# Kernel tuning notes

Measured on AMD Instinct MI355X. Metric: run time of the kernel, lower is better.

## Reference

```python
import jax, jax.numpy as jnp
import numpy as np

PRIMES = (2, 3, 5, 7, 11, 13, 17, 19, 23, 29)
TEMP = 1000.0  # softmax_temperature
B, S = 32, 2048

def _templates(p):
    # circle template for residue r: (cos(2*pi*r/p), sin(2*pi*r/p)) -> [p, 2]
    ang = 2.0 * np.pi * np.arange(p) / p
    return jnp.asarray(np.stack([np.cos(ang), np.sin(ang)], axis=-1).astype(np.float32))

def _mul_onehot(p):
    # onehot[a, b, (a*b) % p] = 1 -> [p, p, p]
    t = (np.arange(p)[:, None] * np.arange(p)[None, :]) % p
    return jnp.asarray((t[..., None] == np.arange(p)).astype(np.float32))

TEMPLATES = [_templates(p) for p in PRIMES]
MUL_OH = [_mul_onehot(p) for p in PRIMES]

def setup_inputs() -> dict:
    key = jax.random.key(0)
    k1, k2 = jax.random.split(key)
    m = len(PRIMES)
    return {
        "a_circle": jax.random.normal(k1, (B, S, m, 2), dtype=jnp.float32),
        "b_circle": jax.random.normal(k2, (B, S, m, 2), dtype=jnp.float32),
    }

def _circle_add(a, b):
    # complex multiply: angles add -> (a + b) mod p on the circle
    ca, sa = a[..., 0], a[..., 1]
    cb, sb = b[..., 0], b[..., 1]
    return jnp.stack([ca * cb - sa * sb, sa * cb + ca * sb], axis=-1)

def _circle_sub(a, b):
    # a - b = a + conj(b): negate sin of b
    b_conj = jnp.stack([b[..., 0], -b[..., 1]], axis=-1)
    return _circle_add(a, b_conj)

def _decode_soft(c_i, tmpl):
    # c_i: [B, S, 2], tmpl: [p, 2] -> soft one-hot over residues [B, S, p]
    sim = jnp.einsum('bsd,pd->bsp', c_i, tmpl)
    return jax.nn.softmax(TEMP * sim, axis=-1)

def _circle_mul(a, b):
    outs = []
    for i, p in enumerate(PRIMES):
        tmpl = TEMPLATES[i]
        a_soft = _decode_soft(a[:, :, i, :], tmpl)
        b_soft = _decode_soft(b[:, :, i, :], tmpl)
        # outer product of soft residues contracted with mul table
        dist = jnp.einsum('bsi,bsj,ijk->bsk', a_soft, b_soft, MUL_OH[i])
        outs.append(dist @ tmpl)  # re-encode to circle: [B, S, 2]
    return jnp.stack(outs, axis=2)  # [B, S, m, 2]

def reference(a_circle, b_circle):
    add = _circle_add(a_circle, b_circle)
    sub = _circle_sub(a_circle, b_circle)
    mul = _circle_mul(a_circle, b_circle)
    return jnp.stack([add, sub, mul], axis=0)  # [3, B, S, m, 2]
```

## Files before the change

### kernel.cpp

```cpp
#include <hip/hip_runtime.h>


#define SOFTMAX_TEMP 1000.0f

constexpr double PI_D = 3.14159265358979323846264338327950288;

constexpr double tay_cos(double x) {
    double x2 = x * x, term = 1.0, sum = 1.0;
    for (int k = 1; k <= 15; ++k) { term *= -x2 / double((2 * k - 1) * (2 * k)); sum += term; }
    return sum;
}
constexpr double tay_sin(double x) {
    double x2 = x * x, term = x, sum = x;
    for (int k = 1; k <= 15; ++k) { term *= -x2 / double((2 * k) * (2 * k + 1)); sum += term; }
    return sum;
}

template <int P> struct Tab { float c[P]; float s[P]; };

template <int P>
constexpr Tab<P> make_tab() {
    Tab<P> t{};
    for (int r = 0; r < P; ++r) {
        double x = 2.0 * PI_D * double(r) / double(P);
        if (x > PI_D) x -= 2.0 * PI_D;
        t.c[r] = (float)tay_cos(x);
        t.s[r] = (float)tay_sin(x);
    }
    return t;
}

template <int P>
__device__ __forceinline__ void mul_prime(float ca, float sa, float cb, float sb,
                                          float& oc, float& os) {
    constexpr Tab<P> T = make_tab<P>();

    float ea[P], eb[P];
    float ma = -1e30f, mb = -1e30f;
#pragma unroll
    for (int r = 0; r < P; ++r) {
        float va = ca * T.c[r] + sa * T.s[r];
        float vb = cb * T.c[r] + sb * T.s[r];
        ea[r] = va; eb[r] = vb;
        ma = fmaxf(ma, va); mb = fmaxf(mb, vb);
    }
    float Sa = 0.f, Sb = 0.f;
#pragma unroll
    for (int r = 0; r < P; ++r) {
        float xa = __expf(SOFTMAX_TEMP * (ea[r] - ma));
        float xb = __expf(SOFTMAX_TEMP * (eb[r] - mb));
        ea[r] = xa; Sa += xa;
        eb[r] = xb; Sb += xb;
    }

    float W[P];
#pragma unroll
    for (int k = 0; k < P; ++k) W[k] = 0.f;
    W[0] = ea[0] * Sb + eb[0] * Sa - ea[0] * eb[0];
#pragma unroll
    for (int i = 1; i < P; ++i) {
#pragma unroll
        for (int j = 1; j < P; ++j) {
            const int k = (i * j) % P;
            W[k] = fmaf(ea[i], eb[j], W[k]);
        }
    }

    float accC = 0.f, accS = 0.f;
#pragma unroll
    for (int k = 0; k < P; ++k) {
        accC = fmaf(W[k], T.c[k], accC);
        accS = fmaf(W[k], T.s[k], accS);
    }
    float inv = 1.0f / (Sa * Sb);
    oc = accC * inv;
    os = accS * inv;
}

__global__ __launch_bounds__(640) void arith_kernel(const float* __restrict__ a,
                                                    const float* __restrict__ b,
                                                    float* __restrict__ out,
                                                    int n_pairs) {
    const int pair = blockIdx.x * 64 + threadIdx.x;
    const int pi = threadIdx.y;
    if (pair >= n_pairs) return;

    const int base = pair * 20 + pi * 2;
    const float2 av = *(const float2*)(a + base);
    const float2 bv = *(const float2*)(b + base);
    const float ca = av.x, sa = av.y, cb = bv.x, sb = bv.y;

    const float pcc = ca * cb, pss = sa * sb, psc = sa * cb, pcs = ca * sb;
    const int plane = n_pairs * 20;
    *(float2*)(out + base)          = make_float2(pcc - pss, psc + pcs);
    *(float2*)(out + plane + base)  = make_float2(pcc + pss, psc - pcs);

    float oc, os;
    switch (pi) {
        case 0: mul_prime<2>(ca, sa, cb, sb, oc, os); break;
        case 1: mul_prime<3>(ca, sa, cb, sb, oc, os); break;
        case 2: mul_prime<5>(ca, sa, cb, sb, oc, os); break;
        case 3: mul_prime<7>(ca, sa, cb, sb, oc, os); break;
        case 4: mul_prime<11>(ca, sa, cb, sb, oc, os); break;
        case 5: mul_prime<13>(ca, sa, cb, sb, oc, os); break;
        case 6: mul_prime<17>(ca, sa, cb, sb, oc, os); break;
        case 7: mul_prime<19>(ca, sa, cb, sb, oc, os); break;
        case 8: mul_prime<23>(ca, sa, cb, sb, oc, os); break;
        default: mul_prime<29>(ca, sa, cb, sb, oc, os); break;
    }
    *(float2*)(out + 2 * plane + base) = make_float2(oc, os);
}

extern "C" void kernel_launch(void* const* d_in, const int* in_sizes, int n_in,
                              void* d_out, int out_size, void* d_ws, size_t ws_size,
                              hipStream_t stream) {
    const float* a = (const float*)d_in[0];
    const float* b = (const float*)d_in[1];
    float* out = (float*)d_out;
    const int n_pairs = in_sizes[0] / 20;

    dim3 block(64, 10);
    dim3 grid((n_pairs + 63) / 64);
    arith_kernel<<<grid, block, 0, stream>>>(a, b, out, n_pairs);
}
```

Measured before the change: 75.95 us.

## Fuse softmax of a into product loop and regroup work into 256-thread blocks

Computes the exponentials of operand a on the fly inside the outer-product loop instead of storing them in an array, and recomputes logits rather than keeping them, which is meant to cut register pressure for large primes. The launch changes from 64x10 blocks to 256-thread blocks, where each 64-lane wavefront handles one (pair-group, prime) unit. This is intended to raise occupancy and scheduling flexibility, at the cost of some recomputed FMAs and extra index arithmetic.

```diff
diff --git a/kernel.cpp b/kernel.cpp
--- a/kernel.cpp
+++ b/kernel.cpp
@@ -35,36 +35,40 @@
                                           float& oc, float& os) {
     constexpr Tab<P> T = make_tab<P>();
 
-    float ea[P], eb[P];
     float ma = -1e30f, mb = -1e30f;
 #pragma unroll
     for (int r = 0; r < P; ++r) {
-        float va = ca * T.c[r] + sa * T.s[r];
-        float vb = cb * T.c[r] + sb * T.s[r];
-        ea[r] = va; eb[r] = vb;
-        ma = fmaxf(ma, va); mb = fmaxf(mb, vb);
+        ma = fmaxf(ma, ca * T.c[r] + sa * T.s[r]);
+        mb = fmaxf(mb, cb * T.c[r] + sb * T.s[r]);
     }
-    float Sa = 0.f, Sb = 0.f;
+
+    float eb[P];
+    float Sb = 0.f;
 #pragma unroll
     for (int r = 0; r < P; ++r) {
-        float xa = __expf(SOFTMAX_TEMP * (ea[r] - ma));
-        float xb = __expf(SOFTMAX_TEMP * (eb[r] - mb));
-        ea[r] = xa; Sa += xa;
-        eb[r] = xb; Sb += xb;
+        float x = __expf(SOFTMAX_TEMP * (cb * T.c[r] + sb * T.s[r] - mb));
+        eb[r] = x; Sb += x;
     }
 
     float W[P];
 #pragma unroll
     for (int k = 0; k < P; ++k) W[k] = 0.f;
-    W[0] = ea[0] * Sb + eb[0] * Sa - ea[0] * eb[0];
+
+    float Sa = 0.f, ea0 = 0.f;
 #pragma unroll
-    for (int i = 1; i < P; ++i) {
+    for (int i = 0; i < P; ++i) {
+        float ea_i = __expf(SOFTMAX_TEMP * (ca * T.c[i] + sa * T.s[i] - ma));
+        Sa += ea_i;
+        if (i == 0) { ea0 = ea_i; }
+        else {
 #pragma unroll
-        for (int j = 1; j < P; ++j) {
-            const int k = (i * j) % P;
-            W[k] = fmaf(ea[i], eb[j], W[k]);
+            for (int j = 1; j < P; ++j) {
+                const int k = (i * j) % P;
+                W[k] = fmaf(ea_i, eb[j], W[k]);
+            }
         }
     }
+    W[0] += ea0 * Sb + eb[0] * (Sa - ea0);
 
     float accC = 0.f, accS = 0.f;
 #pragma unroll
@@ -72,17 +76,21 @@
         accC = fmaf(W[k], T.c[k], accC);
         accS = fmaf(W[k], T.s[k], accS);
     }
-    float inv = 1.0f / (Sa * Sb);
+    const float inv = 1.0f / (Sa * Sb);
     oc = accC * inv;
     os = accS * inv;
 }
 
-__global__ __launch_bounds__(640) void arith_kernel(const float* __restrict__ a,
+__global__ __launch_bounds__(256) void arith_kernel(const float* __restrict__ a,
                                                     const float* __restrict__ b,
                                                     float* __restrict__ out,
-                                                    int n_pairs) {
-    const int pair = blockIdx.x * 64 + threadIdx.x;
-    const int pi = threadIdx.y;
+                                                    int n_pairs, int n_units) {
+    const int lane = threadIdx.x & 63;
+    const int unit = blockIdx.x * 4 + (threadIdx.x >> 6);
+    if (unit >= n_units) return;
+    const int pg = unit / 10;
+    const int pi = unit - pg * 10;
+    const int pair = pg * 64 + lane;
     if (pair >= n_pairs) return;
 
     const int base = pair * 20 + pi * 2;
@@ -92,8 +100,8 @@
 
     const float pcc = ca * cb, pss = sa * sb, psc = sa * cb, pcs = ca * sb;
     const int plane = n_pairs * 20;
-    *(float2*)(out + base)          = make_float2(pcc - pss, psc + pcs);
-    *(float2*)(out + plane + base)  = make_float2(pcc + pss, psc - pcs);
+    *(float2*)(out + base)         = make_float2(pcc - pss, psc + pcs);
+    *(float2*)(out + plane + base) = make_float2(pcc + pss, psc - pcs);
 
     float oc, os;
     switch (pi) {
@@ -118,8 +126,11 @@
     const float* b = (const float*)d_in[1];
     float* out = (float*)d_out;
     const int n_pairs = in_sizes[0] / 20;
+    const int n_groups = (n_pairs + 63) / 64;
+    const int n_units = n_groups * 10;
+    const int n_blocks = (n_units + 3) / 4;
 
-    dim3 block(64, 10);
-    dim3 grid((n_pairs + 63) / 64);
-    arith_kernel<<<grid, block, 0, stream>>>(a, b, out, n_pairs);
+    dim3 block(256);
+    dim3 grid(n_blocks);
+    arith_kernel<<<grid, block, 0, stream>>>(a, b, out, n_pairs, n_units);
 }
```

After: 79.04 us. 1.04x slower.
